# Optimization experiments

Measured on AMD Instinct MI355X. Metric: run time of the kernel, lower is better.

Reference implementation:

```python
import jax, jax.numpy as jnp
import numpy as np

B, N, S, C1, C2 = 8, 8192, 2048, 128, 256
IN_CH = C1 + C2
MLP = [256, 128]
EPS_INTERP = 1e-8
EPS_BN = 1e-5


def setup_inputs() -> dict:
    key = jax.random.key(0)
    ks = jax.random.split(key, 8)
    inp = {
        "xyz1": jax.random.normal(ks[0], (B, 3, N), dtype=jnp.float32),
        "xyz2": jax.random.normal(ks[1], (B, 3, S), dtype=jnp.float32),
        "points1": jax.random.normal(ks[2], (B, C1, N), dtype=jnp.float32),
        "points2": jax.random.normal(ks[3], (B, C2, S), dtype=jnp.float32),
        # Conv1d(k=1) weights as [out, in] matrices, plus BN gamma/beta
        "W1": jax.random.normal(ks[4], (MLP[0], IN_CH), dtype=jnp.float32) * 0.02,
        "b1": jnp.zeros((MLP[0],), dtype=jnp.float32),
        "g1": jnp.ones((MLP[0],), dtype=jnp.float32),
        "be1": jnp.zeros((MLP[0],), dtype=jnp.float32),
        "W2": jax.random.normal(ks[5], (MLP[1], MLP[0]), dtype=jnp.float32) * 0.02,
        "b2": jnp.zeros((MLP[1],), dtype=jnp.float32),
        "g2": jnp.ones((MLP[1],), dtype=jnp.float32),
        "be2": jnp.zeros((MLP[1],), dtype=jnp.float32),
    }
    return inp


def _conv_bn_relu(x, W, b, g, be):
    # x: [B, N, Cin]; 1x1 Conv1d == per-point matmul; BN over (batch, length) per channel (training-mode stats)
    y = jnp.einsum('bnc,oc->bno', x, W) + b
    m = jnp.mean(y, axis=(0, 1))
    v = jnp.var(y, axis=(0, 1))
    return jax.nn.relu((y - m) * jax.lax.rsqrt(v + EPS_BN) * g + be)


def reference(xyz1, xyz2, points1, points2, W1, b1, g1, be1, W2, b2, g2, be2):
    x1 = xyz1.transpose(0, 2, 1)   # [B, N, 3]
    x2 = xyz2.transpose(0, 2, 1)   # [B, S, 3]
    p2 = points2.transpose(0, 2, 1)  # [B, S, C2]
    p1 = points1.transpose(0, 2, 1)  # [B, N, C1]

    # squared pairwise distances [B, N, S]
    d = (jnp.sum(x1 * x1, axis=-1, keepdims=True)
         - 2.0 * jnp.einsum('bnd,bsd->bns', x1, x2)
         + jnp.sum(x2 * x2, axis=-1)[:, None, :])

    # 3 nearest neighbors (smallest distances)
    neg_d, idx = jax.lax.top_k(-d, 3)          # idx: [B, N, 3]
    d3 = -neg_d                                 # [B, N, 3]
    recip = 1.0 / (d3 + EPS_INTERP)
    w = recip / jnp.sum(recip, axis=-1, keepdims=True)  # [B, N, 3]

    gathered = jax.vmap(lambda p, i: p[i])(p2, idx)     # [B, N, 3, C2]
    interp = jnp.sum(gathered * w[..., None], axis=2)   # [B, N, C2]

    x = jnp.concatenate([p1, interp], axis=-1)          # [B, N, C1+C2]
    x = _conv_bn_relu(x, W1, b1, g1, be1)
    x = _conv_bn_relu(x, W2, b2, g2, be2)
    return x.transpose(0, 2, 1)                         # [B, mlp[-1], N]
```

## Files before the change

### kernel.cpp

```cpp
#include <hip/hip_runtime.h>
#include <stdint.h>

#define B_ 8
#define N_ 8192
#define S_ 2048
#define C1_ 128
#define C2_ 256
#define IN_ 384
#define H1_ 256
#define H2_ 128
#define M_ (B_*N_)

typedef short bf16x8 __attribute__((ext_vector_type(8)));
typedef float f32x4 __attribute__((ext_vector_type(4)));

__device__ __forceinline__ float bf2f(unsigned short s){
  union { unsigned int u; float f; } x; x.u = ((unsigned int)s) << 16; return x.f;
}
__device__ __forceinline__ unsigned short f2bf(float f){
  union { float f; unsigned int u; } x; x.f = f;
  unsigned int u = x.u;
  unsigned int r = (u + 0x7FFFu + ((u >> 16) & 1u)) >> 16;
  return (unsigned short)r;
}

__device__ __forceinline__ size_t fragaddr(int m, int k, int K){
  return ((size_t)((m >> 4) * (K >> 5) + (k >> 5)) << 9)
       + (size_t)((((k >> 3) & 3) << 7) + ((m & 15) << 3) + (k & 7));
}

__device__ __forceinline__ void gload_lds16(const unsigned short* g, unsigned short* l){
  __builtin_amdgcn_global_load_lds(
      (const __attribute__((address_space(1))) unsigned int*)g,
      (__attribute__((address_space(3))) unsigned int*)l, 16, 0, 0);
}

#define PIECES_ 8
#define SPP_ (S_ / PIECES_)

__device__ __forceinline__ void insert_k(float& k0, float& k1, float& k2, float x){
  k2 = __builtin_amdgcn_fmed3f(k1, k2, x);
  k1 = __builtin_amdgcn_fmed3f(k0, k1, x);
  k0 = fminf(k0, x);
}

__device__ __forceinline__ void insert3(float& d0, float& d1, float& d2,
                                        int& i0, int& i1, int& i2,
                                        float x, int s){
  bool b0 = x < d0, b1 = x < d1, b2 = x < d2;
  i2 = b1 ? i1 : (b2 ? s : i2);
  i1 = b0 ? i0 : (b1 ? s : i1);
  i0 = b0 ? s : i0;
  d2 = __builtin_amdgcn_fmed3f(d1, d2, x);
  d1 = __builtin_amdgcn_fmed3f(d0, d1, x);
  d0 = fminf(d0, x);
}

__global__ __launch_bounds__(256) void p2t_knn_kernel(
    const float* W1, const float* W2, const float* p2,
    const float* xyz1, const float* xyz2,
    unsigned short* w1b, unsigned short* w2b,
    unsigned short* p2t, float* partd, int* parti)
{
  __shared__ __align__(16) char smraw[4352];
  float (*tile)[33] = reinterpret_cast<float(*)[33]>(smraw);
  float4* pts = reinterpret_cast<float4*>(smraw);
  const int bx = blockIdx.x, t = threadIdx.x;

  if (bx >= 6144){
    int i = (bx - 6144) * 256 + t;
    if (i < 256*384){
      int row = i / 384, col = i - row*384;
      w1b[fragaddr(row, col, 384)] = f2bf(W1[i]);
    }
    if (i < 128*256){
      int row = i >> 8, col = i & 255;
      w2b[fragaddr(row, col, 256)] = f2bf(W2[i]);
    }
    return;
  }

  const int per = bx / 3, r = bx % 3;
  if (r == 0){
    int kid = per;
    int nb = kid & 31, b = (kid >> 5) & 7, piece = kid >> 8;
    int n = nb * 256 + t;
    int base = piece * SPP_;
    const float* x2 = xyz2 + (size_t)b * 3 * S_;
    {
      float px = x2[base + t], py = x2[S_ + base + t], pz = x2[2*S_ + base + t];
      pts[t] = make_float4(-2.f*px, -2.f*py, -2.f*pz, px*px + py*py + pz*pz);
    }
    __syncthreads();
    const float* x1 = xyz1 + (size_t)b * 3 * N_;
    float ax = x1[n], ay = x1[N_ + n], az = x1[2*N_ + n];
    float x1sq = ax*ax + ay*ay + az*az;

    const float KINIT = __uint_as_float(0x7F000000u);
    float ka[3] = {KINIT, KINIT, KINIT};
    float kb[3] = {KINIT, KINIT, KINIT};

    for (int s = 0; s < SPP_; s += 8){
      float4 cb[8];
      #pragma unroll
      for (int u = 0; u < 8; u++) cb[u] = pts[s + u];
      #pragma unroll
      for (int u = 0; u < 8; u++){
        float dd = fmaf(ax, cb[u].x, fmaf(ay, cb[u].y, fmaf(az, cb[u].z, cb[u].w + x1sq)));
        float key = __uint_as_float((__float_as_uint(dd) & 0xFFFFFF00u) | (unsigned)(s + u));
        if (u & 1) insert_k(kb[0], kb[1], kb[2], key);
        else       insert_k(ka[0], ka[1], ka[2], key);
      }
    }
    insert_k(ka[0], ka[1], ka[2], kb[0]);
    insert_k(ka[0], ka[1], ka[2], kb[1]);
    insert_k(ka[0], ka[1], ka[2], kb[2]);

    float ed[3]; int ei[3];
    #pragma unroll
    for (int j = 0; j < 3; j++){
      int li = (int)(__float_as_uint(ka[j]) & 0xFFu);
      float4 c = pts[li];
      float dd = fmaf(ax, c.x, fmaf(ay, c.y, fmaf(az, c.z, c.w + x1sq)));
      ed[j] = fmaxf(dd, 0.f);
      ei[j] = base + li;
    }

    size_t g = (size_t)b * N_ + n;
    partd[(piece*3 + 0)*(size_t)M_ + g] = ed[0];
    partd[(piece*3 + 1)*(size_t)M_ + g] = ed[1];
    partd[(piece*3 + 2)*(size_t)M_ + g] = ed[2];
    parti[(piece*3 + 0)*(size_t)M_ + g] = ei[0];
    parti[(piece*3 + 1)*(size_t)M_ + g] = ei[1];
    parti[(piece*3 + 2)*(size_t)M_ + g] = ei[2];
    return;
  }

  {
    int pid = per*2 + (r - 1);
    int b = pid >> 9, rem = pid & 511;
    int l0 = (rem & 63) * 32, r0 = (rem >> 6) * 32;
    int tx = t & 31, ty = t >> 5;
    const float* src = p2 + (size_t)b * C2_ * S_;
    #pragma unroll
    for (int rr = ty; rr < 32; rr += 8)
      tile[rr][tx] = src[(size_t)(r0 + rr) * S_ + l0 + tx];
    __syncthreads();
    unsigned short* dst = p2t + (size_t)b * S_ * C2_;
    #pragma unroll
    for (int rr = ty; rr < 32; rr += 8)
      dst[(size_t)(l0 + rr) * C2_ + r0 + tx] = f2bf(tile[tx][rr]);
  }
}

__global__ __launch_bounds__(256) void merge_kernel(const float* __restrict__ partd,
                                                    const int* __restrict__ parti,
                                                    int* __restrict__ ibuf,
                                                    float* __restrict__ wbuf){
  size_t g = (size_t)blockIdx.x * 256 + threadIdx.x;
  float d0 = partd[0*(size_t)M_ + g], d1 = partd[1*(size_t)M_ + g], d2 = partd[2*(size_t)M_ + g];
  int   i0 = parti[0*(size_t)M_ + g], i1 = parti[1*(size_t)M_ + g], i2 = parti[2*(size_t)M_ + g];
  #pragma unroll
  for (int p = 1; p < PIECES_; p++)
    #pragma unroll
    for (int j = 0; j < 3; j++)
      insert3(d0, d1, d2, i0, i1, i2,
              partd[(p*3 + j)*(size_t)M_ + g], parti[(p*3 + j)*(size_t)M_ + g]);
  float r0 = 1.f/(d0 + 1e-8f), r1 = 1.f/(d1 + 1e-8f), r2 = 1.f/(d2 + 1e-8f);
  float rs = 1.f/(r0 + r1 + r2);
  ibuf[0*(size_t)M_ + g] = i0;    ibuf[1*(size_t)M_ + g] = i1;    ibuf[2*(size_t)M_ + g] = i2;
  wbuf[0*(size_t)M_ + g] = r0*rs; wbuf[1*(size_t)M_ + g] = r1*rs; wbuf[2*(size_t)M_ + g] = r2*rs;
}

__global__ __launch_bounds__(256) void xbuild_kernel(
    const float* p1, const unsigned short* p2t,
    const int* ibuf, const float* wbuf, unsigned short* x)
{
  __shared__ __align__(16) char smraw[4352];
  float (*tile)[33] = reinterpret_cast<float(*)[33]>(smraw);
  int*   sidx = reinterpret_cast<int*>(smraw);
  float* swgt = reinterpret_cast<float*>(smraw + 192);
  const int bx = blockIdx.x, t = threadIdx.x;
  const int per = bx / 3, r = bx % 3;

  if (r == 0){
    int base = per * 16;
    if (t < 64){
      int q = t >> 2, j = t & 3;
      if (j < 3){
        sidx[q*3 + j] = ibuf[(size_t)j*M_ + base + q];
        swgt[q*3 + j] = wbuf[(size_t)j*M_ + base + q];
      }
    }
    __syncthreads();
    size_t suboff = (size_t)((((t >> 3) & 3) << 7) + (t & 7));
    for (int k = 0; k < 16; k++){
      int g = base + k;
      int b = g >> 13;
      const unsigned short* p = p2t + (size_t)b * S_ * C2_;
      float v = swgt[k*3+0]*bf2f(p[(size_t)sidx[k*3+0]*C2_ + t])
              + swgt[k*3+1]*bf2f(p[(size_t)sidx[k*3+1]*C2_ + t])
              + swgt[k*3+2]*bf2f(p[(size_t)sidx[k*3+2]*C2_ + t]);
      size_t a = ((size_t)((g >> 4)*12 + 4 + (t >> 5)) << 9) + suboff + (size_t)((g & 15) << 3);
      x[a] = f2bf(v);
    }
    return;
  }

  {
    int pid = per*2 + (r - 1);
    int b = pid >> 10, rem = pid & 1023;
    int l0 = (rem & 255) * 32, r0 = (rem >> 8) * 32;
    int tx = t & 31, ty = t >> 5;
    const float* src = p1 + (size_t)b * C1_ * N_;
    #pragma unroll
    for (int rr = ty; rr < 32; rr += 8)
      tile[rr][tx] = src[(size_t)(r0 + rr) * N_ + l0 + tx];
    __syncthreads();
    #pragma unroll
    for (int rr = ty; rr < 32; rr += 8){
      int g = b * N_ + l0 + rr;
      size_t a = ((size_t)((g >> 4)*12 + (r0 >> 5)) << 9)
               + (size_t)((((tx >> 3) & 3) << 7) + ((g & 15) << 3) + (tx & 7));
      x[a] = f2bf(tile[tx][rr]);
    }
  }
}

__device__ __forceinline__ bf16x8 bn_relu_frag(bf16x8 v, const float* a, const float* c, int kb){
  union { bf16x8 h; unsigned short s[8]; } u; u.h = v;
  union { float4 v4; float f[4]; } a0, a1, c0, c1;
  a0.v4 = *(const float4*)(a + kb);  a1.v4 = *(const float4*)(a + kb + 4);
  c0.v4 = *(const float4*)(c + kb);  c1.v4 = *(const float4*)(c + kb + 4);
  #pragma unroll
  for (int j = 0; j < 4; j++){
    float f0 = fmaf(a0.f[j], bf2f(u.s[j]),     c0.f[j]);
    float f1 = fmaf(a1.f[j], bf2f(u.s[j + 4]), c1.f[j]);
    u.s[j]     = f2bf(fmaxf(f0, 0.f));
    u.s[j + 4] = f2bf(fmaxf(f1, 0.f));
  }
  return u.h;
}

template<int K, bool HAS_AFF, bool OUT_FRAG>
__global__ __launch_bounds__(256) void gemm_lds_kernel(
    const unsigned short* __restrict__ A, const unsigned short* __restrict__ Wf,
    unsigned short* __restrict__ Cout, int Ntot,
    float* pbuf, const float* aff_a, const float* aff_c)
{
  constexpr int KT = K / 32;
  __shared__ unsigned short smA[128*64];
  __shared__ unsigned short smB[128*64];
  __shared__ float ldsStat[256];

  const int t = threadIdx.x;
  const int lane = t & 63, wave = t >> 6;
  const int ln = lane & 15, lq = lane >> 4;
  const int wm = wave >> 1, wn = wave & 1;
  const int mtb = blockIdx.x * 8;
  const int ntb = blockIdx.y * 8;
  const int mtw = mtb + wm * 4;
  const int n0  = blockIdx.y * 128 + wn * 64;

  ldsStat[t] = 0.f;

  const int c0 = 2*wave, c1 = 2*wave + 1;

  const f32x4 fzero = {0.f, 0.f, 0.f, 0.f};
  f32x4 acc[4][4];
  #pragma unroll
  for (int i = 0; i < 4; i++)
    #pragma unroll
    for (int j = 0; j < 4; j++) acc[i][j] = fzero;

  for (int kk = 0; kk < KT; kk += 2){
    #pragma unroll
    for (int q = 0; q < 2; q++){
      gload_lds16(A  + (((size_t)((mtb + c0)*KT + kk + q)) << 9) + lane*8,
                  &smA[((c0*2 + q) << 9) + lane*8]);
      gload_lds16(A  + (((size_t)((mtb + c1)*KT + kk + q)) << 9) + lane*8,
                  &smA[((c1*2 + q) << 9) + lane*8]);
      gload_lds16(Wf + (((size_t)((ntb + c0)*KT + kk + q)) << 9) + lane*8,
                  &smB[((c0*2 + q) << 9) + lane*8]);
      gload_lds16(Wf + (((size_t)((ntb + c1)*KT + kk + q)) << 9) + lane*8,
                  &smB[((c1*2 + q) << 9) + lane*8]);
    }
    __syncthreads();
    #pragma unroll
    for (int q = 0; q < 2; q++){
      bf16x8 af[4], bfr[4];
      #pragma unroll
      for (int i = 0; i < 4; i++)
        af[i] = *(const bf16x8*)(&smA[(((wm*4 + i)*2 + q) << 9) + lane*8]);
      #pragma unroll
      for (int j = 0; j < 4; j++)
        bfr[j] = *(const bf16x8*)(&smB[(((wn*4 + j)*2 + q) << 9) + lane*8]);
      if (HAS_AFF){
        const int kb = (kk + q)*32 + lq*8;
        #pragma unroll
        for (int i = 0; i < 4; i++) af[i] = bn_relu_frag(af[i], aff_a, aff_c, kb);
      }
      #pragma unroll
      for (int i = 0; i < 4; i++)
        #pragma unroll
        for (int j = 0; j < 4; j++)
          acc[i][j] = __builtin_amdgcn_mfma_f32_16x16x32_bf16(af[i], bfr[j], acc[i][j], 0, 0, 0);
    }
    __syncthreads();
  }

  #pragma unroll
  for (int j = 0; j < 4; j++){
    int ncol = n0 + j*16 + ln;
    float s = 0.f, q = 0.f;
    #pragma unroll
    for (int i = 0; i < 4; i++){
      #pragma unroll
      for (int r = 0; r < 4; r++){
        float v = acc[i][j][r];
        if (OUT_FRAG){
          size_t a = ((size_t)((mtw + i)*8 + (ncol >> 5)) << 9)
                   + (size_t)((((ncol >> 3) & 3) << 7) + ((lq*4 + r) << 3) + (ncol & 7));
          Cout[a] = f2bf(v);
        } else {
          Cout[((size_t)((mtw + i)*16 + lq*4 + r)) * Ntot + ncol] = f2bf(v);
        }
        s += v; q += v*v;
      }
    }
    s += __shfl_xor(s, 16); s += __shfl_xor(s, 32);
    q += __shfl_xor(q, 16); q += __shfl_xor(q, 32);
    if (lq == 0){
      int colLocal = wn*64 + j*16 + ln;
      atomicAdd(&ldsStat[colLocal], s);
      atomicAdd(&ldsStat[128 + colLocal], q);
    }
  }
  __syncthreads();
  pbuf[((size_t)(blockIdx.y * gridDim.x + blockIdx.x) << 8) + t] = ldsStat[t];
}

__global__ __launch_bounds__(256) void finalize_kernel(const float* pbuf, const float* g,
                                                       const float* be, float* a_out,
                                                       float* c_out){
  __shared__ float red[8];
  int c = blockIdx.x, t = threadIdx.x;
  int grp = c >> 7, lc = c & 127;
  const float* base = pbuf + ((size_t)(grp * 512) << 8);
  float s = base[((size_t)t << 8) + lc]       + base[((size_t)(t + 256) << 8) + lc];
  float q = base[((size_t)t << 8) + 128 + lc] + base[((size_t)(t + 256) << 8) + 128 + lc];
  #pragma unroll
  for (int o = 1; o < 64; o <<= 1){ s += __shfl_xor(s, o); q += __shfl_xor(q, o); }
  int w = t >> 6;
  if ((t & 63) == 0){ red[w] = s; red[4 + w] = q; }
  __syncthreads();
  if (t == 0){
    s = red[0] + red[1] + red[2] + red[3];
    q = red[4] + red[5] + red[6] + red[7];
    float mean = s * (1.f / M_);
    float var  = q * (1.f / M_) - mean*mean;
    float a = g[c] * rsqrtf(var + 1e-5f);
    a_out[c] = a;
    c_out[c] = fmaf(-mean, a, be[c]);
  }
}

__global__ __launch_bounds__(256) void out_kernel(const unsigned short* y2, const float* a2,
                                                  const float* c2, float* out){
  __shared__ float lds[64][65];
  int t  = threadIdx.x;
  int b  = blockIdx.z;
  int n0 = blockIdx.y * 64;
  int c0 = blockIdx.x * 64;
  int cc = t & 63, tr = t >> 6;
  float a = a2[c0 + cc], cadd = c2[c0 + cc];
  #pragma unroll
  for (int ph = 0; ph < 16; ph++){
    int nr = tr + ph*4;
    unsigned short v = y2[((size_t)(b*N_ + n0 + nr)) * H2_ + c0 + cc];
    lds[nr][cc] = fmaxf(fmaf(a, bf2f(v), cadd), 0.f);
  }
  __syncthreads();
  #pragma unroll
  for (int ph = 0; ph < 16; ph++){
    int cr = tr + ph*4;
    out[((size_t)(b*H2_ + c0 + cr)) * N_ + n0 + cc] = lds[cc][cr];
  }
}

extern "C" void kernel_launch(void* const* d_in, const int* in_sizes, int n_in,
                              void* d_out, int out_size, void* d_ws, size_t ws_size,
                              hipStream_t stream){
  const float* xyz1 = (const float*)d_in[0];
  const float* xyz2 = (const float*)d_in[1];
  const float* p1   = (const float*)d_in[2];
  const float* p2   = (const float*)d_in[3];
  const float* W1   = (const float*)d_in[4];
  const float* g1   = (const float*)d_in[6];
  const float* be1  = (const float*)d_in[7];
  const float* W2   = (const float*)d_in[8];
  const float* g2   = (const float*)d_in[10];
  const float* be2  = (const float*)d_in[11];
  float* out = (float*)d_out;

  char* ws = (char*)d_ws;
  unsigned short* x    = (unsigned short*)(ws + 0);
  unsigned short* p2t  = (unsigned short*)(ws + 50331648);
  unsigned short* y1   = (unsigned short*)(ws + 58720256);
  unsigned short* y2   = (unsigned short*)(ws + 92274688);
  unsigned short* w1b  = (unsigned short*)(ws + 109051904);
  unsigned short* w2b  = (unsigned short*)(ws + 109248512);
  float*          stats= (float*)(ws + 110886912);
  float* a1   = stats + 768;  float* c1  = stats + 1024;
  float* a2   = stats + 1280; float* c2  = stats + 1408;
  float* partd = (float*)y1;
  int*   parti = (int*)(y1 + 6291456);
  int*   ibuf = (int*)  (ws + 58720256 + 20971520);
  float* wbuf = (float*)(ws + 58720256 + 23068672);
  float* pbuf1 = (float*)p2t;
  float* pbuf2 = (float*)x;

  p2t_knn_kernel<<<6528, 256, 0, stream>>>(W1, W2, p2, xyz1, xyz2, w1b, w2b, p2t, partd, parti);
  merge_kernel<<<256, 256, 0, stream>>>(partd, parti, ibuf, wbuf);
  xbuild_kernel<<<12288, 256, 0, stream>>>(p1, p2t, ibuf, wbuf, x);
  gemm_lds_kernel<384, false, true><<<dim3(512, 2), 256, 0, stream>>>(
      x, w1b, y1, 256, pbuf1, nullptr, nullptr);
  finalize_kernel<<<256, 256, 0, stream>>>(pbuf1, g1, be1, a1, c1);
  gemm_lds_kernel<256, true, false><<<dim3(512, 1), 256, 0, stream>>>(
      y1, w2b, y2, 128, pbuf2, a1, c1);
  finalize_kernel<<<128, 256, 0, stream>>>(pbuf2, g2, be2, a2, c2);
  out_kernel<<<dim3(2, 128, 8), 256, 0, stream>>>(y2, a2, c2, out);
}
```

Baseline: 254.6 us.

## Vectorize interpolation gather and rebalance knn/transpose block interleaving

The interpolation path now has each wavefront handle one point and each lane load four consecutive bf16 channels with a single 8-byte load, writing four outputs as one vector store. Before, every thread handled one channel across all 16 points using scalar 2-byte loads and stores. Separately, the fused knn/transpose kernel no longer assigns blocks in a 1:2 ratio via bx/3. It alternates knn and p2 transpose blocks one-to-one in the first 4096 blocks and runs the remaining transpose blocks afterwards. This aims to cut memory instruction count and rebalance the workload mix across CUs.

```diff
diff --git a/kernel.cpp b/kernel.cpp
--- a/kernel.cpp
+++ b/kernel.cpp
@@ -13,6 +13,8 @@
 
 typedef short bf16x8 __attribute__((ext_vector_type(8)));
 typedef float f32x4 __attribute__((ext_vector_type(4)));
+typedef short short4v __attribute__((ext_vector_type(4)));
+typedef unsigned short ushort4v __attribute__((ext_vector_type(4)));
 
 __device__ __forceinline__ float bf2f(unsigned short s){
   union { unsigned int u; float f; } x; x.u = ((unsigned int)s) << 16; return x.f;
@@ -80,9 +82,16 @@
     return;
   }
 
-  const int per = bx / 3, r = bx % 3;
-  if (r == 0){
-    int kid = per;
+  int knnId = -1, p2tId;
+  if (bx < 4096){
+    if ((bx & 1) == 0) knnId = bx >> 1;
+    else               p2tId = bx >> 1;
+  } else {
+    p2tId = 2048 + (bx - 4096);
+  }
+
+  if (knnId >= 0){
+    int kid = knnId;
     int nb = kid & 31, b = (kid >> 5) & 7, piece = kid >> 8;
     int n = nb * 256 + t;
     int base = piece * SPP_;
@@ -137,7 +146,7 @@
   }
 
   {
-    int pid = per*2 + (r - 1);
+    int pid = p2tId;
     int b = pid >> 9, rem = pid & 511;
     int l0 = (rem & 63) * 32, r0 = (rem >> 6) * 32;
     int tx = t & 31, ty = t >> 5;
@@ -193,16 +202,29 @@
       }
     }
     __syncthreads();
-    size_t suboff = (size_t)((((t >> 3) & 3) << 7) + (t & 7));
-    for (int k = 0; k < 16; k++){
+    const int wv = t >> 6, ln = t & 63;
+    #pragma unroll
+    for (int kq = 0; kq < 4; kq++){
+      int k = kq*4 + wv;
       int g = base + k;
       int b = g >> 13;
       const unsigned short* p = p2t + (size_t)b * S_ * C2_;
-      float v = swgt[k*3+0]*bf2f(p[(size_t)sidx[k*3+0]*C2_ + t])
-              + swgt[k*3+1]*bf2f(p[(size_t)sidx[k*3+1]*C2_ + t])
-              + swgt[k*3+2]*bf2f(p[(size_t)sidx[k*3+2]*C2_ + t]);
-      size_t a = ((size_t)((g >> 4)*12 + 4 + (t >> 5)) << 9) + suboff + (size_t)((g & 15) << 3);
-      x[a] = f2bf(v);
+      float a0 = 0.f, a1 = 0.f, a2 = 0.f, a3 = 0.f;
+      #pragma unroll
+      for (int j = 0; j < 3; j++){
+        ushort4v v = *(const ushort4v*)(p + (size_t)sidx[k*3+j]*C2_ + 4*ln);
+        float w = swgt[k*3+j];
+        a0 = fmaf(w, bf2f(v[0]), a0);
+        a1 = fmaf(w, bf2f(v[1]), a1);
+        a2 = fmaf(w, bf2f(v[2]), a2);
+        a3 = fmaf(w, bf2f(v[3]), a3);
+      }
+      short4v o;
+      o[0] = (short)f2bf(a0); o[1] = (short)f2bf(a1);
+      o[2] = (short)f2bf(a2); o[3] = (short)f2bf(a3);
+      size_t a = ((size_t)((g >> 4)*12 + 4 + (ln >> 3)) << 9)
+               + (size_t)((((ln >> 1) & 3) << 7) + ((g & 15) << 3) + ((ln & 1) * 4));
+      *(short4v*)(x + a) = o;
     }
     return;
   }
```

New measurement: 263.6 us. 3.5% more time.
